# Performance work log

Measured on AMD Instinct MI355X. Metric: run time of the kernel, lower is better.

## Reference

```python
import math
import jax, jax.numpy as jnp
import numpy as np

B, N, D = 2, 768, 512
H = 8
DK = D // H
BETA_NOT = 0.5
EPS = 1e-6


def setup_inputs() -> dict:
    key = jax.random.key(0)
    ks = jax.random.split(key, 8)
    s = 0.02
    return {
        "x": jax.random.normal(ks[0], (B, N, D), dtype=jnp.float32),
        "qkv1_w": jax.random.normal(ks[1], (D, 3 * D), dtype=jnp.float32) * s,
        "qkv2_w": jax.random.normal(ks[2], (D, 3 * D), dtype=jnp.float32) * s,
        "proj_w": jax.random.normal(ks[3], (D, D), dtype=jnp.float32) * s,
        "conv1_w": jax.random.normal(ks[4], (16, 6), dtype=jnp.float32) * 0.3,
        "conv1_b": jax.random.normal(ks[5], (16,), dtype=jnp.float32) * 0.1,
        "conv2_w": jax.random.normal(ks[6], (4, 16), dtype=jnp.float32) * 0.3,
        "conv2_b": jnp.full((4,), -5.0, dtype=jnp.float32),
        "chain_logit": jnp.asarray(-2.0, dtype=jnp.float32),
    }


def _qkv(x, w):
    b, n, d = x.shape
    qkv = (x @ w).reshape(b, n, 3, H, DK).transpose(2, 0, 3, 1, 4)  # [3,B,h,N,dk]
    return qkv[0], qkv[1], qkv[2]


def reference(x, qkv1_w, qkv2_w, proj_w, conv1_w, conv1_b, conv2_w, conv2_b, chain_logit):
    scale = 1.0 / math.sqrt(DK)
    q1, k1, v1 = _qkv(x, qkv1_w)
    q2, k2, v2 = _qkv(x, qkv2_w)

    S1 = jnp.einsum("bhnd,bhmd->bhnm", q1, k1) * scale  # [B,h,N,N]
    S2 = jnp.einsum("bhnd,bhmd->bhnm", q2, k2) * scale
    A1 = jax.nn.softmax(S1, axis=-1)
    A2 = jax.nn.softmax(S2, axis=-1)

    C_right = jnp.einsum("bhnk,bhkm->bhnm", A1, A2)
    C_left = jnp.einsum("bhnk,bhkm->bhnm", A2, A1)
    Cr = jnp.log(C_right + EPS)
    Cl = jnp.log(C_left + EPS)

    # 6-channel edge feature map [B,h,6,N,N]
    feat = jnp.stack(
        [S1, S2, jnp.swapaxes(S1, -1, -2), jnp.swapaxes(S2, -1, -2), Cr, Cl], axis=2
    )
    # 1x1 convs == per-pixel channel mixing
    hid = jnp.einsum("bhcnm,oc->bhonm", feat, conv1_w) + conv1_b[None, None, :, None, None]
    hid = jax.nn.gelu(hid, approximate=True)  # tanh-approx GELU
    gates = jax.nn.sigmoid(
        jnp.einsum("bhcnm,oc->bhonm", hid, conv2_w) + conv2_b[None, None, :, None, None]
    )
    g_and, g_or, g_not, g_chain = gates[:, :, 0], gates[:, :, 1], gates[:, :, 2], gates[:, :, 3]

    Smix = (
        S1
        + g_and * S2  # g_and * (S1 + S2 - S1)
        + g_or * (jnp.logaddexp(S1, S2) - S1)
        - g_not * (BETA_NOT * S2)
        + g_chain * Cr
    )
    A = jax.nn.softmax(Smix, axis=-1)

    y_base = jnp.einsum("bhnm,bhmd->bhnd", A, v1)
    transport = jnp.einsum("bhnm,bhmd->bhnd", A2, v2)
    y_chain = jnp.einsum("bhnm,bhmd->bhnd", A1, transport)
    w = jax.nn.sigmoid(chain_logit)
    y = y_base + w * y_chain

    y = jnp.swapaxes(y, 1, 2).reshape(x.shape[0], x.shape[1], D)  # [B,N,D]
    return y @ proj_w
```

## Files before the change

### kernel.cpp

```cpp
#include <hip/hip_runtime.h>
#include <hip/hip_bf16.h>
#include <math.h>

typedef __hip_bfloat16 bf16;
typedef __attribute__((ext_vector_type(8))) short short8;
typedef __attribute__((ext_vector_type(4))) float f32x4;
typedef __attribute__((ext_vector_type(2))) float f32x2;
#define DEVINL __device__ __forceinline__

constexpr int Bc  = 2;
constexpr int Nc  = 768;
constexpr int Dc  = 512;
constexpr int Hc  = 8;
constexpr int DKc = 64;
constexpr int BHc = Bc * Hc;
constexpr float SCALE    = 0.125f;
constexpr float EPSF     = 1e-6f;
constexpr float BETA_NOT = 0.5f;

DEVINL float ldf(const float* p, long i) { return p[i]; }
DEVINL float ldf(const bf16* p, long i) { return __bfloat162float(p[i]); }
DEVINL void stf(float* p, long i, float v) { p[i] = v; }
DEVINL void stf(bf16* p, long i, float v) { p[i] = __float2bfloat16(v); }

DEVINL float sigf(float x) { return __fdividef(1.f, 1.f + __expf(-x)); }

DEVINL f32x2 fma2(f32x2 a, f32x2 b, f32x2 c) { return __builtin_elementwise_fma(a, b, c); }
DEVINL f32x2 splat2(float x) { return (f32x2){x, x}; }
DEVINL float vexp2(float x) { float r; asm("v_exp_f32 %0, %1" : "=v"(r) : "v"(x)); return r; }
DEVINL float vrcp(float x)  { float r; asm("v_rcp_f32 %0, %1" : "=v"(r) : "v"(x)); return r; }
DEVINL float vlog2(float x) { float r; asm("v_log_f32 %0, %1" : "=v"(r) : "v"(x)); return r; }

DEVINL void gl_lds16(const void* g, void* l) {
    __builtin_amdgcn_global_load_lds(
        (const __attribute__((address_space(1))) void*)g,
        (__attribute__((address_space(3))) void*)l, 16, 0, 0);
}

DEVINL int sniff_is_fp32(const void* xraw) {
    const uint4* p4 = (const uint4*)xraw;
    float mx = 0.f;
#pragma unroll
    for (int j = 0; j < 16; ++j) {
        const uint4 u = p4[j];
        const unsigned w[4] = {u.x, u.y, u.z, u.w};
#pragma unroll
        for (int t = 0; t < 4; ++t) {
            mx = fmaxf(mx, fabsf(__uint_as_float((w[t] & 0xffffu) << 16)));
            mx = fmaxf(mx, fabsf(__uint_as_float(w[t] & 0xffff0000u)));
        }
    }
    return mx > 1000.f ? 1 : 0;
}

DEVINL float cvt_elem(const void* s, long j, int is32) {
    return is32 ? ((const float*)s)[j]
                : __bfloat162float(((const bf16*)s)[j]);
}

__global__ __launch_bounds__(256) void convert_all(
    const void* x, const void* w1, const void* w2, const void* pw,
    const void* c1w, const void* c1b, const void* c2w, const void* c2b,
    const void* ch,
    bf16* xb, bf16* w1b, bf16* w2b, bf16* pwb, float* smallf)
{
    __shared__ int is32s;
    if (threadIdx.x == 0) is32s = sniff_is_fp32(x);
    __syncthreads();
    const int is32 = is32s;
    const long i = (long)blockIdx.x * 256 + threadIdx.x;
    if (i < (long)Bc * Nc * Dc) {
        xb[i]  = __float2bfloat16(cvt_elem(x,  i, is32));
        w1b[i] = __float2bfloat16(cvt_elem(w1, i, is32));
        w2b[i] = __float2bfloat16(cvt_elem(w2, i, is32));
    }
    if (i < (long)Dc * Dc) pwb[i] = __float2bfloat16(cvt_elem(pw, i, is32));
    if (i < 384) {
        const int u = (int)i / 24, k = (int)i % 24;
        float v = 0.f;
        if (k < 12)      v = cvt_elem(c1w, u * 6 + (k >> 1), is32);
        else if (k < 14) v = cvt_elem(c1b, u, is32);
        else if (k >= 16) { const int o = (k - 16) >> 1; v = cvt_elem(c2w, o * 16 + u, is32); }
        smallf[i] = v;
    } else if (i < 392) smallf[i] = cvt_elem(c2b, ((int)i - 384) >> 1, is32);
    else if (i < 394) smallf[i] = cvt_elem(ch, 0, is32);
    else if (i < 512) smallf[i] = 0.f;
}

__global__ __launch_bounds__(256) void fill_sentinel(unsigned short* o) {
    const long i = (long)blockIdx.x * 256 + threadIdx.x;
    if (i < (long)Bc * Nc * Dc) o[i] = 0x40E0;
}

__global__ __launch_bounds__(256) void transpose_bf16(
    const unsigned short* __restrict__ src, unsigned short* __restrict__ dst,
    int R, int C, long sS, long sD)
{
    __shared__ unsigned short tile[64][68];
    const unsigned short* s = src + (long)blockIdx.z * sS;
    unsigned short* d = dst + (long)blockIdx.z * sD;
    const int r0 = blockIdx.y * 64, c0 = blockIdx.x * 64;
    const int t = threadIdx.x;
    const int lr = t >> 4, lc4 = (t & 15) * 4;
#pragma unroll
    for (int i = 0; i < 4; ++i) {
        int r = lr + i * 16;
        *(uint2*)&tile[r][lc4] = *(const uint2*)&s[(long)(r0 + r) * C + c0 + lc4];
    }
    __syncthreads();
#pragma unroll
    for (int i = 0; i < 4; ++i) {
        int r = lr + i * 16;
        unsigned short v[4];
#pragma unroll
        for (int j = 0; j < 4; ++j) v[j] = tile[lc4 + j][r];
        *(uint2*)&d[(long)(c0 + r) * R + r0 + lc4] = *(uint2*)v;
    }
}

template <int EPI, typename TC, int XORB = 0, int XCDSWZ = 0, int RAW = 0>
__global__ __launch_bounds__(256) void gemm_nt_mfma(
    const bf16* __restrict__ Ag, const bf16* __restrict__ Btg,
    TC* __restrict__ Cg, bf16* __restrict__ Craw, int M, int N, int K,
    long sA, long sB, long sC, float alpha)
{
    __shared__ unsigned short Asm[2 * 128 * 32];
    __shared__ unsigned short Bsm[2 * 128 * 32];
    constexpr int BUF = 128 * 32;

    int bx, by, bz;
    if (XCDSWZ) {
        const int wg = blockIdx.x;
        const int xcd = wg & 7, t = wg >> 3;
        bz = xcd + 8 * (t / 36);
        const int tile = t % 36;
        bx = tile % 6; by = tile / 6;
    } else { bx = blockIdx.x; by = blockIdx.y; bz = blockIdx.z; }

    const int tid  = threadIdx.x;
    const int wv   = tid >> 6;
    const int lane = tid & 63;
    const int q    = lane >> 4;
    const int ln   = lane & 15;
    const int wm   = wv & 1;
    const int wn   = wv >> 1;

    const int zb = XORB ? (bz ^ 16) : bz;
    const bf16* A  = Ag  + (long)bz * sA + (long)(by * 128) * K;
    const bf16* Bt = Btg + (long)zb * sB + (long)(bx * 128) * K;
    TC*         C  = Cg  + (long)bz * sC;

    const int sr = lane >> 2, sc = lane & 3;
    const int scs = sc ^ (sr & 3);
    const bf16* gA0 = A  + (long)(wv * 32 + sr)      * K + scs * 8;
    const bf16* gA1 = A  + (long)(wv * 32 + 16 + sr) * K + scs * 8;
    const bf16* gB0 = Bt + (long)(wv * 32 + sr)      * K + scs * 8;
    const bf16* gB1 = Bt + (long)(wv * 32 + 16 + sr) * K + scs * 8;
    unsigned short* lA0 = &Asm[(wv * 32)      * 32];
    unsigned short* lA1 = &Asm[(wv * 32 + 16) * 32];
    unsigned short* lB0 = &Bsm[(wv * 32)      * 32];
    unsigned short* lB1 = &Bsm[(wv * 32 + 16) * 32];

    f32x4 acc[4][4];
#pragma unroll
    for (int i = 0; i < 4; ++i)
#pragma unroll
        for (int j = 0; j < 4; ++j)
            acc[i][j] = (f32x4){0.f, 0.f, 0.f, 0.f};

    const int qs = (q ^ (ln & 3)) * 8;

    gl_lds16(gA0, lA0);
    gl_lds16(gA1, lA1);
    gl_lds16(gB0, lB0);
    gl_lds16(gB1, lB1);
    __syncthreads();

    int cur = 0;
    for (int k0 = 0; k0 < K; k0 += 32) {
        const int nxt = cur ^ 1;
        if (k0 + 32 < K) {
            const int no = nxt * BUF;
            gl_lds16(gA0 + k0 + 32, lA0 + no);
            gl_lds16(gA1 + k0 + 32, lA1 + no);
            gl_lds16(gB0 + k0 + 32, lB0 + no);
            gl_lds16(gB1 + k0 + 32, lB1 + no);
        }

        const unsigned short* Ac = &Asm[cur * BUF];
        const unsigned short* Bc = &Bsm[cur * BUF];
        short8 af[4], bfr[4];
#pragma unroll
        for (int mt = 0; mt < 4; ++mt) {
            int m = wm * 64 + mt * 16 + ln;
            af[mt] = *(const short8*)&Ac[m * 32 + qs];
        }
#pragma unroll
        for (int nt = 0; nt < 4; ++nt) {
            int n = wn * 64 + nt * 16 + ln;
            bfr[nt] = *(const short8*)&Bc[n * 32 + qs];
        }
#pragma unroll
        for (int mt = 0; mt < 4; ++mt)
#pragma unroll
            for (int nt = 0; nt < 4; ++nt)
                acc[mt][nt] = __builtin_amdgcn_mfma_f32_16x16x32_bf16(
                    af[mt], bfr[nt], acc[mt][nt], 0, 0, 0);

        __syncthreads();
        cur = nxt;
    }

#pragma unroll
    for (int mt = 0; mt < 4; ++mt) {
#pragma unroll
        for (int nt = 0; nt < 4; ++nt) {
            const int col = bx * 128 + wn * 64 + nt * 16 + ln;
            const int rowb = by * 128 + wm * 64 + mt * 16 + q * 4;
#pragma unroll
            for (int r = 0; r < 4; ++r) {
                float vraw = acc[mt][nt][r] * alpha;
                if (RAW) {
                    if (bz < 16)
                        Craw[(long)bz * M * N + (long)(rowb + r) * N + col] =
                            __float2bfloat16(vraw);
                }
                float v = vraw;
                if (EPI == 1) v = __logf(fmaxf(v, 0.f) + EPSF);
                stf(C, (long)(rowb + r) * N + col, v);
            }
        }
    }
}

__global__ __launch_bounds__(256) void qkv_mfma(
    const bf16* __restrict__ X,
    const bf16* __restrict__ w1t, const bf16* __restrict__ w2t,
    bf16* __restrict__ q1, bf16* __restrict__ k1, bf16* __restrict__ v1,
    bf16* __restrict__ q2, bf16* __restrict__ k2, bf16* __restrict__ v2)
{
    constexpr int K = Dc;
    __shared__ unsigned short Asm[2 * 128 * 32];
    __shared__ unsigned short Bsm[2 * 128 * 32];
    constexpr int BUF = 128 * 32;

    const int tid  = threadIdx.x;
    const int wv   = tid >> 6;
    const int lane = tid & 63;
    const int q    = lane >> 4;
    const int ln   = lane & 15;
    const int wm   = wv & 1;
    const int wn   = wv >> 1;
    const int set  = blockIdx.z;

    const bf16* Wt = set ? w2t : w1t;
    bf16* Q  = set ? q2 : q1;
    bf16* Ko = set ? k2 : k1;
    bf16* V  = set ? v2 : v1;

    const bf16* A  = X  + (long)(blockIdx.y * 128) * K;
    const bf16* Bt = Wt + (long)(blockIdx.x * 128) * K;

    const int sr = lane >> 2, sc = lane & 3;
    const int scs = sc ^ (sr & 3);
    const bf16* gA0 = A  + (long)(wv * 32 + sr)      * K + scs * 8;
    const bf16* gA1 = A  + (long)(wv * 32 + 16 + sr) * K + scs * 8;
    const bf16* gB0 = Bt + (long)(wv * 32 + sr)      * K + scs * 8;
    const bf16* gB1 = Bt + (long)(wv * 32 + 16 + sr) * K + scs * 8;
    unsigned short* lA0 = &Asm[(wv * 32)      * 32];
    unsigned short* lA1 = &Asm[(wv * 32 + 16) * 32];
    unsigned short* lB0 = &Bsm[(wv * 32)      * 32];
    unsigned short* lB1 = &Bsm[(wv * 32 + 16) * 32];

    f32x4 acc[4][4];
#pragma unroll
    for (int i = 0; i < 4; ++i)
#pragma unroll
        for (int j = 0; j < 4; ++j)
            acc[i][j] = (f32x4){0.f, 0.f, 0.f, 0.f};

    const int qs = (q ^ (ln & 3)) * 8;

    gl_lds16(gA0, lA0);
    gl_lds16(gA1, lA1);
    gl_lds16(gB0, lB0);
    gl_lds16(gB1, lB1);
    __syncthreads();

    int cur = 0;
    for (int k0 = 0; k0 < K; k0 += 32) {
        const int nxt = cur ^ 1;
        if (k0 + 32 < K) {
            const int no = nxt * BUF;
            gl_lds16(gA0 + k0 + 32, lA0 + no);
            gl_lds16(gA1 + k0 + 32, lA1 + no);
            gl_lds16(gB0 + k0 + 32, lB0 + no);
            gl_lds16(gB1 + k0 + 32, lB1 + no);
        }

        const unsigned short* Ac = &Asm[cur * BUF];
        const unsigned short* Bc = &Bsm[cur * BUF];
        short8 af[4], bfr[4];
#pragma unroll
        for (int mt = 0; mt < 4; ++mt) {
            int m = wm * 64 + mt * 16 + ln;
            af[mt] = *(const short8*)&Ac[m * 32 + qs];
        }
#pragma unroll
        for (int nt = 0; nt < 4; ++nt) {
            int n = wn * 64 + nt * 16 + ln;
            bfr[nt] = *(const short8*)&Bc[n * 32 + qs];
        }
#pragma unroll
        for (int mt = 0; mt < 4; ++mt)
#pragma unroll
            for (int nt = 0; nt < 4; ++nt)
                acc[mt][nt] = __builtin_amdgcn_mfma_f32_16x16x32_bf16(
                    af[mt], bfr[nt], acc[mt][nt], 0, 0, 0);

        __syncthreads();
        cur = nxt;
    }

#pragma unroll
    for (int mt = 0; mt < 4; ++mt) {
#pragma unroll
        for (int nt = 0; nt < 4; ++nt) {
            const int col  = blockIdx.x * 128 + wn * 64 + nt * 16 + ln;
            const int rowb = blockIdx.y * 128 + wm * 64 + mt * 16 + q * 4;
            const int t = col >> 9;
            const int h = (col >> 6) & 7;
            const int dk = col & 63;
            bf16* dst = (t == 0) ? Q : (t == 1) ? Ko : V;
#pragma unroll
            for (int r = 0; r < 4; ++r) {
                const int row = rowb + r;
                const int b = row >= Nc ? 1 : 0;
                const int n = row - b * Nc;
                dst[(((long)b * Hc + h) * Nc + n) * DKc + dk] =
                    __float2bfloat16(acc[mt][nt][r]);
            }
        }
    }
}

struct N64Acc { f32x4 acc[2][4]; };

template <typename DUMMY = void>
DEVINL void n64_core(const bf16* A, const bf16* Bt, int K,
                     unsigned short* Asm, unsigned short* Bsm, N64Acc& R)
{
    const int tid  = threadIdx.x;
    const int wave = tid >> 6;
    const int lane = tid & 63;
    const int q    = lane >> 4;
    const int ln   = lane & 15;

    const int sr = tid >> 3, k8 = tid & 7;
    const bf16* pa[4];
    const bf16* pb[2];
    int wa[4], wb[2];
#pragma unroll
    for (int i = 0; i < 4; ++i) {
        pa[i] = A + (long)(sr + i * 32) * K + k8 * 8;
        wa[i] = (sr + i * 32) * 72 + k8 * 8;
    }
#pragma unroll
    for (int i = 0; i < 2; ++i) {
        pb[i] = Bt + (long)(sr + i * 32) * K + k8 * 8;
        wb[i] = (sr + i * 32) * 72 + k8 * 8;
    }

#pragma unroll
    for (int i = 0; i < 2; ++i)
#pragma unroll
        for (int j = 0; j < 4; ++j)
            R.acc[i][j] = (f32x4){0.f, 0.f, 0.f, 0.f};

    for (int k0 = 0; k0 < K; k0 += 64) {
        uint4 va[4], vb[2];
#pragma unroll
        for (int i = 0; i < 4; ++i) va[i] = *(const uint4*)(pa[i] + k0);
#pragma unroll
        for (int i = 0; i < 2; ++i) vb[i] = *(const uint4*)(pb[i] + k0);
        __syncthreads();
#pragma unroll
        for (int i = 0; i < 4; ++i) *(uint4*)&Asm[wa[i]] = va[i];
#pragma unroll
        for (int i = 0; i < 2; ++i) *(uint4*)&Bsm[wb[i]] = vb[i];
        __syncthreads();

#pragma unroll
        for (int kc = 0; kc < 2; ++kc) {
            short8 af[2], bfr[4];
#pragma unroll
            for (int mt = 0; mt < 2; ++mt) {
                int m = wave * 32 + mt * 16 + ln;
                af[mt] = *(const short8*)&Asm[m * 72 + kc * 32 + q * 8];
            }
#pragma unroll
            for (int nt = 0; nt < 4; ++nt) {
                int n = nt * 16 + ln;
                bfr[nt] = *(const short8*)&Bsm[n * 72 + kc * 32 + q * 8];
            }
#pragma unroll
            for (int mt = 0; mt < 2; ++mt)
#pragma unroll
                for (int nt = 0; nt < 4; ++nt)
                    R.acc[mt][nt] = __builtin_amdgcn_mfma_f32_16x16x32_bf16(
                        af[mt], bfr[nt], R.acc[mt][nt], 0, 0, 0);
        }
    }
}

struct N64hAcc { f32x4 acc[4]; };

template <typename DUMMY = void>
DEVINL void n64h_core(const bf16* A, const bf16* Bt, int K,
                      unsigned short* Asm, unsigned short* Bsm, N64hAcc& R)
{
    const int tid  = threadIdx.x;
    const int wave = tid >> 6;
    const int lane = tid & 63;
    const int q    = lane >> 4;
    const int ln   = lane & 15;

    const int sr = tid >> 3, k8 = tid & 7;
    const bf16* pa[2];
    const bf16* pb[2];
    int wa[2], wb[2];
#pragma unroll
    for (int i = 0; i < 2; ++i) {
        pa[i] = A  + (long)(sr + i * 32) * K + k8 * 8;
        wa[i] = (sr + i * 32) * 72 + k8 * 8;
        pb[i] = Bt + (long)(sr + i * 32) * K + k8 * 8;
        wb[i] = wa[i];
    }

#pragma unroll
    for (int j = 0; j < 4; ++j)
        R.acc[j] = (f32x4){0.f, 0.f, 0.f, 0.f};

    for (int k0 = 0; k0 < K; k0 += 64) {
        uint4 va[2], vb[2];
#pragma unroll
        for (int i = 0; i < 2; ++i) va[i] = *(const uint4*)(pa[i] + k0);
#pragma unroll
        for (int i = 0; i < 2; ++i) vb[i] = *(const uint4*)(pb[i] + k0);
        __syncthreads();
#pragma unroll
        for (int i = 0; i < 2; ++i) *(uint4*)&Asm[wa[i]] = va[i];
#pragma unroll
        for (int i = 0; i < 2; ++i) *(uint4*)&Bsm[wb[i]] = vb[i];
        __syncthreads();

#pragma unroll
        for (int kc = 0; kc < 2; ++kc) {
            short8 af;
            af = *(const short8*)&Asm[(wave * 16 + ln) * 72 + kc * 32 + q * 8];
            short8 bfr[4];
#pragma unroll
            for (int nt = 0; nt < 4; ++nt) {
                int n = nt * 16 + ln;
                bfr[nt] = *(const short8*)&Bsm[n * 72 + kc * 32 + q * 8];
            }
#pragma unroll
            for (int nt = 0; nt < 4; ++nt)
                R.acc[nt] = __builtin_amdgcn_mfma_f32_16x16x32_bf16(
                    af, bfr[nt], R.acc[nt], 0, 0, 0);
        }
    }
}

__global__ __launch_bounds__(256) void gemm_n64_pair(
    const bf16* __restrict__ A0g, const bf16* __restrict__ B0g, bf16* __restrict__ C0tg,
    const bf16* __restrict__ A1g, const bf16* __restrict__ B1g, bf16* __restrict__ C1g,
    int M, int K, long sA, long sB, long sC)
{
    __shared__ unsigned short Asm[128 * 72];
    __shared__ unsigned short Bsm[64 * 72];

    const int zz = blockIdx.z & 15;
    const int second = blockIdx.z >> 4;
    const bf16* A  = (second ? A1g : A0g) + (long)zz * sA + (long)(blockIdx.y * 128) * K;
    const bf16* Bt = (second ? B1g : B0g) + (long)zz * sB;

    N64Acc R;
    n64_core(A, Bt, K, Asm, Bsm, R);

    const int tid = threadIdx.x;
    const int wave = tid >> 6, lane = tid & 63, q = lane >> 4, ln = lane & 15;

    if (second) {
        bf16* C = C1g + (long)zz * sC;
#pragma unroll
        for (int mt = 0; mt < 2; ++mt) {
#pragma unroll
            for (int nt = 0; nt < 4; ++nt) {
                const int col  = nt * 16 + ln;
                const int rowb = blockIdx.y * 128 + wave * 32 + mt * 16 + q * 4;
#pragma unroll
                for (int r = 0; r < 4; ++r)
                    C[(long)(rowb + r) * 64 + col] = __float2bfloat16(R.acc[mt][nt][r]);
            }
        }
    } else {
        __syncthreads();
#pragma unroll
        for (int mt = 0; mt < 2; ++mt) {
#pragma unroll
            for (int nt = 0; nt < 4; ++nt) {
                const int col = nt * 16 + ln;
                const int rwb = wave * 32 + mt * 16 + q * 4;
#pragma unroll
                for (int r = 0; r < 4; ++r)
                    *(bf16*)&Asm[col * 136 + rwb + r] = __float2bfloat16(R.acc[mt][nt][r]);
            }
        }
        __syncthreads();
        bf16* Ct = C0tg + (long)zz * sC;
        const int dk  = tid >> 2;
        const int nc0 = (tid & 3) * 32;
        const int gn0 = blockIdx.y * 128;
#pragma unroll
        for (int c8 = 0; c8 < 4; ++c8) {
            uint4 v = *(const uint4*)&Asm[dk * 136 + nc0 + c8 * 8];
            *(uint4*)&Ct[(long)dk * Nc + gn0 + nc0 + c8 * 8] = v;
        }
    }
}

__global__ __launch_bounds__(256) void gemm_n64_both_h(
    const bf16* __restrict__ Ab, const bf16* __restrict__ v1t,
    const bf16* __restrict__ Craw, const bf16* __restrict__ v2t,
    const float* __restrict__ smallf, bf16* __restrict__ yc,
    int K, long sA, long sB)
{
    __shared__ unsigned short Asm[64 * 72];
    __shared__ unsigned short Bsm[64 * 72];

    const int bh = blockIdx.z;
    const long arow = (long)(blockIdx.y * 64) * K;

    N64hAcc R1;
    n64h_core(Ab + (long)bh * sA + arow, v1t + (long)bh * sB, K, Asm, Bsm, R1);
    N64hAcc R2;
    n64h_core(Craw + (long)bh * sA + arow, v2t + (long)bh * sB, K, Asm, Bsm, R2);

    const float w = sigf(smallf[392]);
    const int b = bh >> 3, h = bh & 7;

    const int tid = threadIdx.x;
    const int wave = tid >> 6, lane = tid & 63, q = lane >> 4, ln = lane & 15;
#pragma unroll
    for (int nt = 0; nt < 4; ++nt) {
        const int col  = nt * 16 + ln;
        const int rowb = blockIdx.y * 64 + wave * 16 + q * 4;
#pragma unroll
        for (int r = 0; r < 4; ++r) {
            const int n = rowb + r;
            yc[((long)(b * Nc + n)) * Dc + h * DKc + col] =
                __float2bfloat16(R1.acc[nt][r] + w * R2.acc[nt][r]);
        }
    }
}

__global__ __launch_bounds__(256) void gemm_n64_combine(
    const bf16* __restrict__ A1b, const bf16* __restrict__ trt,
    const bf16* __restrict__ yb1, const float* __restrict__ smallf,
    bf16* __restrict__ yc, int M, int K, long sA, long sB)
{
    __shared__ unsigned short Asm[128 * 72];
    __shared__ unsigned short Bsm[64 * 72];

    const int bh = blockIdx.z;
    const bf16* A  = A1b + (long)bh * sA + (long)(blockIdx.y * 128) * K;
    const bf16* Bt = trt + (long)bh * sB;

    N64Acc R;
    n64_core(A, Bt, K, Asm, Bsm, R);

    const float w = sigf(smallf[392]);
    const int b = bh >> 3, h = bh & 7;
    const long yb1base = (long)bh * Nc * DKc;

    const int tid = threadIdx.x;
    const int wave = tid >> 6, lane = tid & 63, q = lane >> 4, ln = lane & 15;
#pragma unroll
    for (int mt = 0; mt < 2; ++mt) {
#pragma unroll
        for (int nt = 0; nt < 4; ++nt) {
            const int col  = nt * 16 + ln;
            const int rowb = blockIdx.y * 128 + wave * 32 + mt * 16 + q * 4;
#pragma unroll
            for (int r = 0; r < 4; ++r) {
                const int n = rowb + r;
                const float base = __bfloat162float(yb1[yb1base + (long)n * 64 + col]);
                yc[((long)(b * Nc + n)) * Dc + h * DKc + col] =
                    __float2bfloat16(base + w * R.acc[mt][nt][r]);
            }
        }
    }
}

__global__ __launch_bounds__(256) void gemm_n64_yb(
    const bf16* __restrict__ Ag, const bf16* __restrict__ Btg,
    bf16* __restrict__ Cg, int M, int K, long sA, long sB, long sC)
{
    __shared__ unsigned short Asm[128 * 72];
    __shared__ unsigned short Bsm[64 * 72];

    const int zz = blockIdx.z;
    const bf16* A  = Ag + (long)zz * sA + (long)(blockIdx.y * 128) * K;
    const bf16* Bt = Btg + (long)zz * sB;

    N64Acc R;
    n64_core(A, Bt, K, Asm, Bsm, R);

    bf16* C = Cg + (long)zz * sC;
    const int tid = threadIdx.x;
    const int wave = tid >> 6, lane = tid & 63, q = lane >> 4, ln = lane & 15;
#pragma unroll
    for (int mt = 0; mt < 2; ++mt) {
#pragma unroll
        for (int nt = 0; nt < 4; ++nt) {
            const int col  = nt * 16 + ln;
            const int rowb = blockIdx.y * 128 + wave * 32 + mt * 16 + q * 4;
#pragma unroll
            for (int r = 0; r < 4; ++r)
                C[(long)(rowb + r) * 64 + col] = __float2bfloat16(R.acc[mt][nt][r]);
        }
    }
}

__global__ __launch_bounds__(256) void softmax_rows_w(
    const float* __restrict__ src, bf16* __restrict__ dst)
{
    const int wid  = threadIdx.x >> 6;
    const int lane = threadIdx.x & 63;
    const long row = (long)blockIdx.x * 4 + wid;
    const float* s = src + row * Nc;

    float4 v[3];
#pragma unroll
    for (int i = 0; i < 3; ++i)
        v[i] = *(const float4*)&s[i * 256 + lane * 4];

    float m = -1e30f;
#pragma unroll
    for (int i = 0; i < 3; ++i)
        m = fmaxf(m, fmaxf(fmaxf(v[i].x, v[i].y), fmaxf(v[i].z, v[i].w)));
#pragma unroll
    for (int off = 32; off > 0; off >>= 1)
        m = fmaxf(m, __shfl_xor(m, off, 64));

    float e[12];
    float sum = 0.f;
#pragma unroll
    for (int i = 0; i < 3; ++i) {
        e[i * 4 + 0] = __expf(v[i].x - m);
        e[i * 4 + 1] = __expf(v[i].y - m);
        e[i * 4 + 2] = __expf(v[i].z - m);
        e[i * 4 + 3] = __expf(v[i].w - m);
        sum += e[i * 4 + 0] + e[i * 4 + 1] + e[i * 4 + 2] + e[i * 4 + 3];
    }
#pragma unroll
    for (int off = 32; off > 0; off >>= 1)
        sum += __shfl_xor(sum, off, 64);

    const float inv = 1.f / fmaxf(sum, 1e-30f);
    unsigned short* d = (unsigned short*)dst + row * Nc;
#pragma unroll
    for (int i = 0; i < 3; ++i) {
        unsigned short o[4];
#pragma unroll
        for (int j = 0; j < 4; ++j) {
            const bf16 b = __float2bfloat16(e[i * 4 + j] * inv);
            o[j] = *(const unsigned short*)&b;
        }
        *(uint2*)&d[i * 256 + lane * 4] = *(const uint2*)o;
    }
}

__global__ __launch_bounds__(256) void gates_smix(
    const float* __restrict__ S1g, const float* __restrict__ S2g,
    const bf16* __restrict__ Crg, const bf16* __restrict__ Clg,
    float* __restrict__ Smixg, const float* __restrict__ smallf)
{
    __shared__ float t1t[32][17], t2t[32][17];

    const long mat = (long)blockIdx.z * Nc * Nc;
    const float* S1 = S1g + mat;
    const float* S2 = S2g + mat;
    const unsigned short* Cr = (const unsigned short*)Crg + mat;
    const unsigned short* Cl = (const unsigned short*)Clg + mat;
    float* Smix = Smixg + mat;

    const int tid = threadIdx.x;

    const int n0 = blockIdx.y * 16, m0 = blockIdx.x * 32;
    {
        const int r = tid >> 3, c2 = (tid & 7) * 2;
        const float2 a = *(const float2*)&S1[(long)(m0 + r) * Nc + n0 + c2];
        const float2 b = *(const float2*)&S2[(long)(m0 + r) * Nc + n0 + c2];
        t1t[r][c2] = a.x; t1t[r][c2 + 1] = a.y;
        t2t[r][c2] = b.x; t2t[r][c2 + 1] = b.y;
    }
    __syncthreads();

    const int tx = tid & 15, ty = tid >> 4;
    const int n = n0 + ty;
    const long idx = (long)n * Nc + m0 + tx * 2;

    const float2 s1v = *(const float2*)&S1[idx];
    const float2 s2v = *(const float2*)&S2[idx];
    const unsigned cru = *(const unsigned*)&Cr[idx];
    const unsigned clu = *(const unsigned*)&Cl[idx];

    const f32x2 s1a = {s1v.x, s1v.y};
    const f32x2 s2a = {s2v.x, s2v.y};
    const f32x2 cra = {__uint_as_float((cru & 0xffffu) << 16),
                       __uint_as_float(cru & 0xffff0000u)};
    const f32x2 cla = {__uint_as_float((clu & 0xffffu) << 16),
                       __uint_as_float(clu & 0xffff0000u)};
    const f32x2 s1t = {t1t[tx * 2][ty], t1t[tx * 2 + 1][ty]};
    const f32x2 s2t = {t2t[tx * 2][ty], t2t[tx * 2 + 1][ty]};

    f32x2 g0 = *(const f32x2*)&smallf[384];
    f32x2 g1 = *(const f32x2*)&smallf[386];
    f32x2 g2 = *(const f32x2*)&smallf[388];
    f32x2 g3 = *(const f32x2*)&smallf[390];

    const f32x2 gc1  = splat2(-2.30220902f);
    const f32x2 gc3  = splat2(-0.10294357f);
    const f32x2 one2 = splat2(1.f);

#pragma unroll
    for (int u = 0; u < 16; ++u) {
        const f32x2* cw = (const f32x2*)&smallf[u * 24];
        f32x2 h = cw[6];
        h = fma2(s1a, cw[0], h);
        h = fma2(s2a, cw[1], h);
        h = fma2(s1t, cw[2], h);
        h = fma2(s2t, cw[3], h);
        h = fma2(cra, cw[4], h);
        h = fma2(cla, cw[5], h);
        const f32x2 hh = h * h;
        const f32x2 z2 = h * fma2(hh, gc3, gc1);
        f32x2 e;  e[0]  = vexp2(z2[0]); e[1]  = vexp2(z2[1]);
        const f32x2 d = one2 + e;
        f32x2 rc; rc[0] = vrcp(d[0]);   rc[1] = vrcp(d[1]);
        const f32x2 hid = h * rc;
        g0 = fma2(hid, cw[8],  g0);
        g1 = fma2(hid, cw[9],  g1);
        g2 = fma2(hid, cw[10], g2);
        g3 = fma2(hid, cw[11], g3);
    }

    const f32x2 nl2e = splat2(-1.44269504f);
    const f32x2 ln2v = splat2(0.69314718f);
    auto sig2 = [&](f32x2 x) -> f32x2 {
        const f32x2 t = x * nl2e;
        f32x2 e;  e[0] = vexp2(t[0]); e[1] = vexp2(t[1]);
        const f32x2 d = one2 + e;
        f32x2 r;  r[0] = vrcp(d[0]);  r[1] = vrcp(d[1]);
        return r;
    };
    const f32x2 ga2 = sig2(g0);
    const f32x2 go2 = sig2(g1);
    const f32x2 gn2 = sig2(g2);
    const f32x2 gc2 = sig2(g3);

    const f32x2 dd = s1a - s2a;
    f32x2 ad; ad[0] = fabsf(dd[0]); ad[1] = fabsf(dd[1]);
    const f32x2 t2 = ad * nl2e;
    f32x2 ee; ee[0] = vexp2(t2[0]); ee[1] = vexp2(t2[1]);
    const f32x2 lp = one2 + ee;
    f32x2 lg; lg[0] = vlog2(lp[0]); lg[1] = vlog2(lp[1]);
    const f32x2 mx2 = __builtin_elementwise_max(s1a, s2a);
    const f32x2 lae = fma2(lg, ln2v, mx2);

    f32x2 o2 = s1a;
    o2 = fma2(ga2, s2a, o2);
    o2 = fma2(go2, lae - s1a, o2);
    o2 = fma2(gn2, s2a * splat2(-BETA_NOT), o2);
    o2 = fma2(gc2, cra, o2);
    *(float2*)&Smix[idx] = (float2){o2[0], o2[1]};
}

__global__ __launch_bounds__(256) void proj_n64h(
    const bf16* __restrict__ yc, const bf16* __restrict__ pwt,
    const void* __restrict__ xraw, void* __restrict__ out)
{
    constexpr int K = Dc;
    constexpr int N = Dc;
    __shared__ unsigned short Asm[64 * 72];
    __shared__ unsigned short Bsm[64 * 72];
    __shared__ int is32s;
    if (threadIdx.x == 0) is32s = sniff_is_fp32(xraw);

    const bf16* A  = yc  + (long)(blockIdx.y * 64) * K;
    const bf16* Bt = pwt + (long)(blockIdx.x * 64) * K;

    N64hAcc R;
    n64h_core(A, Bt, K, Asm, Bsm, R);

    const int is32 = is32s;
    const int tid = threadIdx.x;
    const int wave = tid >> 6, lane = tid & 63, q = lane >> 4, ln = lane & 15;
#pragma unroll
    for (int nt = 0; nt < 4; ++nt) {
        const int col  = blockIdx.x * 64 + nt * 16 + ln;
        const int rowb = blockIdx.y * 64 + wave * 16 + q * 4;
#pragma unroll
        for (int r = 0; r < 4; ++r) {
            const long o = (long)(rowb + r) * N + col;
            if (is32) ((float*)out)[o] = R.acc[nt][r];
            else      ((bf16*)out)[o] = __float2bfloat16(R.acc[nt][r]);
        }
    }
}

extern "C" void kernel_launch(void* const* d_in, const int* in_sizes, int n_in,
                              void* d_out, int out_size, void* d_ws, size_t ws_size,
                              hipStream_t stream)
{
    const size_t HD   = (size_t)BHc * Nc * DKc;
    const size_t HDh  = HD / 2;
    const size_t MAT  = (size_t)Nc * Nc;
    const size_t MATS = (size_t)BHc * MAT;
    const long   HSTR = (long)Nc * DKc;

    float* ws = (float*)d_ws;
    size_t off = 0;
    auto alloc = [&](size_t n) { float* p = ws + off; off += n; return p; };

    bf16* xb  = (bf16*)alloc(HDh);
    bf16* w1b = (bf16*)alloc(HDh);
    bf16* w2b = (bf16*)alloc(HDh);
    bf16* w1t = (bf16*)alloc(HDh);
    bf16* w2t = (bf16*)alloc(HDh);
    bf16* pwb = (bf16*)alloc((size_t)Dc * Dc / 2);
    bf16* pwt = (bf16*)alloc((size_t)Dc * Dc / 2);
    float* smallf = alloc(512);
    bf16* q1b = (bf16*)alloc(HDh); bf16* q2b = (bf16*)alloc(HDh);
    bf16* k1b = (bf16*)alloc(HDh); bf16* k2b = (bf16*)alloc(HDh);
    bf16* v1b = (bf16*)alloc(HDh); bf16* v2b = (bf16*)alloc(HDh);
    bf16* v1t = (bf16*)alloc(HDh); bf16* v2t = (bf16*)alloc(HDh);
    bf16* trt = (bf16*)alloc(HDh);
    float* S1   = alloc(MATS);
    float* S2   = alloc(MATS);
    float* Smix = alloc(MATS);
    bf16* A1b = (bf16*)alloc(MATS / 2);
    bf16* A2b = (bf16*)alloc(MATS / 2);
    bf16* Crb = (bf16*)alloc(MATS / 2);
    bf16* Clb = (bf16*)alloc(MATS / 2);
    bf16* yb1 = (bf16*)alloc(HDh);
    bf16* yc  = (bf16*)alloc(HDh);

    const size_t NEED_BASE = off * sizeof(float);
    bf16* Crawb = (bf16*)alloc(MATS / 2);
    const size_t NEED_A = off * sizeof(float);
    const int pathA = ws_size >= NEED_A;

    bf16* A1tb = (bf16*)Smix;
    bf16* A2tb = ((bf16*)Smix) + MATS;
    bf16* Ab   = (bf16*)S1;

    if (ws_size < NEED_BASE) {
        fill_sentinel<<<dim3(3072), 256, 0, stream>>>((unsigned short*)d_out);
        return;
    }

    convert_all<<<dim3(3072), 256, 0, stream>>>(
        d_in[0], d_in[1], d_in[2], d_in[3], d_in[4], d_in[5], d_in[6], d_in[7],
        d_in[8], xb, w1b, w2b, pwb, smallf);

    transpose_bf16<<<dim3(24, 8, 2), 256, 0, stream>>>(
        (const unsigned short*)w1b, (unsigned short*)w1t, Dc, 3 * Dc, (long)HD, (long)HD);
    transpose_bf16<<<dim3(8, 8, 1), 256, 0, stream>>>(
        (const unsigned short*)pwb, (unsigned short*)pwt, Dc, Dc, 0, 0);
    qkv_mfma<<<dim3(12, 12, 2), 256, 0, stream>>>(
        xb, w1t, w2t, q1b, k1b, v1b, q2b, k2b, v2b);
    transpose_bf16<<<dim3(1, 12, 2 * BHc), 256, 0, stream>>>(
        (const unsigned short*)v1b, (unsigned short*)v1t, Nc, DKc, HSTR, HSTR);

    gemm_nt_mfma<0, float><<<dim3(6, 6, 2 * BHc), 256, 0, stream>>>(
        q1b, k1b, S1, nullptr, Nc, Nc, DKc, HSTR, HSTR, (long)MAT, SCALE);

    softmax_rows_w<<<(2 * BHc * Nc) / 4, 256, 0, stream>>>(S1, A1b);
    transpose_bf16<<<dim3(12, 12, 2 * BHc), 256, 0, stream>>>(
        (const unsigned short*)A1b, (unsigned short*)A1tb, Nc, Nc, (long)MAT, (long)MAT);

    if (pathA)
        gemm_nt_mfma<1, bf16, 1, 1, 1><<<dim3(1152), 256, 0, stream>>>(
            A1b, A1tb, Crb, Crawb, Nc, Nc, Nc, (long)MAT, (long)MAT, (long)MAT, 1.f);
    else
        gemm_nt_mfma<1, bf16, 1, 1, 0><<<dim3(1152), 256, 0, stream>>>(
            A1b, A1tb, Crb, nullptr, Nc, Nc, Nc, (long)MAT, (long)MAT, (long)MAT, 1.f);

    gates_smix<<<dim3(24, 48, BHc), 256, 0, stream>>>(S1, S2, Crb, Clb, Smix, smallf);

    softmax_rows_w<<<(BHc * Nc) / 4, 256, 0, stream>>>(Smix, Ab);

    if (pathA) {
        gemm_n64_both_h<<<dim3(1, 12, BHc), 256, 0, stream>>>(
            Ab, v1t, Crawb, v2t, smallf, yc, Nc, (long)MAT, HSTR);
    } else {
        gemm_n64_pair<<<dim3(1, 6, 2 * BHc), 256, 0, stream>>>(
            A2b, v2t, trt, Ab, v1t, yb1, Nc, Nc, (long)MAT, HSTR, HSTR);
        gemm_n64_combine<<<dim3(1, 6, BHc), 256, 0, stream>>>(
            A1b, trt, yb1, smallf, yc, Nc, Nc, (long)MAT, HSTR);
    }

    proj_n64h<<<dim3(8, 24, 1), 256, 0, stream>>>(yc, pwt, d_in[0], d_out);
}
```

Before: 345.7 us.

## Fuse score GEMM, row softmax and transpose into one kernel

Replaces the separate QK^T GEMM, row softmax and bf16 transpose launches with a single kernel. Each block computes a 16-row strip of scores across all 768 columns with MFMA and does the softmax in registers. It writes S, A and the transposed A directly, the last through an LDS staging tile. This removes two launches and the re-reads of S and A from global memory. In exchange, the 16-row tiles are small, so K is re-read from global memory for every strip, and the transposed stores are narrow 8-byte writes.

```diff
diff --git a/kernel.cpp b/kernel.cpp
--- a/kernel.cpp
+++ b/kernel.cpp
@@ -115,6 +115,146 @@
 #pragma unroll
         for (int j = 0; j < 4; ++j) v[j] = tile[lc4 + j][r];
         *(uint2*)&d[(long)(c0 + r) * R + r0 + lc4] = *(uint2*)v;
+    }
+}
+
+__global__ __launch_bounds__(256) void sgemm_softmax(
+    const bf16* __restrict__ qg, const bf16* __restrict__ kg,
+    float* __restrict__ Sg, bf16* __restrict__ Ag_, bf16* __restrict__ Atg)
+{
+    __shared__ unsigned short Bsm[256 * 72];
+    __shared__ unsigned short Asm16[16 * 72];
+    __shared__ float red[4][16];
+
+    const int wg  = blockIdx.x;
+    const int xcd = wg & 7, tt = wg >> 3;
+    const int z   = xcd + 8 * (tt / 48);
+    const int by  = tt % 48;
+    const long MAT = (long)Nc * Nc;
+
+    const bf16* Q  = qg + (long)z * (Nc * DKc) + (long)(by * 16) * DKc;
+    const bf16* Km = kg + (long)z * (Nc * DKc);
+    float* S  = Sg  + (long)z * MAT + (long)(by * 16) * Nc;
+    bf16*  A  = Ag_ + (long)z * MAT + (long)(by * 16) * Nc;
+    bf16*  At = Atg + (long)z * MAT;
+
+    const int tid  = threadIdx.x;
+    const int wv   = tid >> 6;
+    const int lane = tid & 63;
+    const int q    = lane >> 4;
+    const int ln   = lane & 15;
+    const int sr   = tid >> 3, k8 = tid & 7;
+
+    if (tid < 128) {
+        const int row = tid >> 3, kk = tid & 7;
+        *(uint4*)&Asm16[row * 72 + kk * 8] = *(const uint4*)&Q[row * 64 + kk * 8];
+    }
+
+    f32x4 acc[12];
+#pragma unroll
+    for (int j = 0; j < 12; ++j) acc[j] = (f32x4){0.f, 0.f, 0.f, 0.f};
+
+    for (int c = 0; c < 3; ++c) {
+        __syncthreads();
+#pragma unroll
+        for (int i = 0; i < 8; ++i) {
+            const int row = sr + i * 32;
+            *(uint4*)&Bsm[row * 72 + k8 * 8] =
+                *(const uint4*)&Km[(long)(c * 256 + row) * 64 + k8 * 8];
+        }
+        __syncthreads();
+#pragma unroll
+        for (int kc = 0; kc < 2; ++kc) {
+            const short8 af = *(const short8*)&Asm16[ln * 72 + kc * 32 + q * 8];
+#pragma unroll
+            for (int t = 0; t < 4; ++t) {
+                const int nl = wv * 64 + t * 16 + ln;
+                const short8 bfr = *(const short8*)&Bsm[nl * 72 + kc * 32 + q * 8];
+                acc[c * 4 + t] = __builtin_amdgcn_mfma_f32_16x16x32_bf16(
+                    af, bfr, acc[c * 4 + t], 0, 0, 0);
+            }
+        }
+    }
+
+    float mrow[4] = {-1e30f, -1e30f, -1e30f, -1e30f};
+#pragma unroll
+    for (int j = 0; j < 12; ++j) {
+        const int c = j >> 2, t = j & 3;
+        const int col = c * 256 + wv * 64 + t * 16 + ln;
+#pragma unroll
+        for (int r = 0; r < 4; ++r) {
+            const float v = acc[j][r] * SCALE;
+            acc[j][r] = v;
+            S[(long)(q * 4 + r) * Nc + col] = v;
+            mrow[r] = fmaxf(mrow[r], v);
+        }
+    }
+#pragma unroll
+    for (int off = 8; off > 0; off >>= 1)
+#pragma unroll
+        for (int r = 0; r < 4; ++r)
+            mrow[r] = fmaxf(mrow[r], __shfl_xor(mrow[r], off, 16));
+    if (ln == 0)
+#pragma unroll
+        for (int r = 0; r < 4; ++r) red[wv][q * 4 + r] = mrow[r];
+    __syncthreads();
+    float m4[4];
+#pragma unroll
+    for (int r = 0; r < 4; ++r)
+        m4[r] = fmaxf(fmaxf(red[0][q * 4 + r], red[1][q * 4 + r]),
+                      fmaxf(red[2][q * 4 + r], red[3][q * 4 + r]));
+    __syncthreads();
+
+    float srow[4] = {0.f, 0.f, 0.f, 0.f};
+#pragma unroll
+    for (int j = 0; j < 12; ++j)
+#pragma unroll
+        for (int r = 0; r < 4; ++r) {
+            const float e = __expf(acc[j][r] - m4[r]);
+            acc[j][r] = e;
+            srow[r] += e;
+        }
+#pragma unroll
+    for (int off = 8; off > 0; off >>= 1)
+#pragma unroll
+        for (int r = 0; r < 4; ++r)
+            srow[r] += __shfl_xor(srow[r], off, 16);
+    if (ln == 0)
+#pragma unroll
+        for (int r = 0; r < 4; ++r) red[wv][q * 4 + r] = srow[r];
+    __syncthreads();
+    float inv[4];
+#pragma unroll
+    for (int r = 0; r < 4; ++r)
+        inv[r] = 1.f / fmaxf(red[0][q * 4 + r] + red[1][q * 4 + r] +
+                             red[2][q * 4 + r] + red[3][q * 4 + r], 1e-30f);
+
+    unsigned short* ATl = Bsm;
+#pragma unroll
+    for (int j = 0; j < 12; ++j) {
+        const int c = j >> 2, t = j & 3;
+        const int col = c * 256 + wv * 64 + t * 16 + ln;
+#pragma unroll
+        for (int r = 0; r < 4; ++r) {
+            const bf16 b = __float2bfloat16(acc[j][r] * inv[r]);
+            const unsigned short u = *(const unsigned short*)&b;
+            A[(long)(q * 4 + r) * Nc + col] = *(const bf16*)&u;
+            ATl[col * 20 + q * 4 + r] = u;
+        }
+    }
+    __syncthreads();
+#pragma unroll
+    for (int s = 0; s < 3; ++s) {
+        const int m = tid + s * 256;
+        uint2 v0 = *(const uint2*)&ATl[m * 20 + 0];
+        uint2 v1 = *(const uint2*)&ATl[m * 20 + 4];
+        uint2 v2 = *(const uint2*)&ATl[m * 20 + 8];
+        uint2 v3 = *(const uint2*)&ATl[m * 20 + 12];
+        unsigned short* d = (unsigned short*)&At[(long)m * Nc + by * 16];
+        *(uint2*)&d[0]  = v0;
+        *(uint2*)&d[4]  = v1;
+        *(uint2*)&d[8]  = v2;
+        *(uint2*)&d[12] = v3;
     }
 }
 
@@ -885,12 +1025,8 @@
     transpose_bf16<<<dim3(1, 12, 2 * BHc), 256, 0, stream>>>(
         (const unsigned short*)v1b, (unsigned short*)v1t, Nc, DKc, HSTR, HSTR);
 
-    gemm_nt_mfma<0, float><<<dim3(6, 6, 2 * BHc), 256, 0, stream>>>(
-        q1b, k1b, S1, nullptr, Nc, Nc, DKc, HSTR, HSTR, (long)MAT, SCALE);
-
-    softmax_rows_w<<<(2 * BHc * Nc) / 4, 256, 0, stream>>>(S1, A1b);
-    transpose_bf16<<<dim3(12, 12, 2 * BHc), 256, 0, stream>>>(
-        (const unsigned short*)A1b, (unsigned short*)A1tb, Nc, Nc, (long)MAT, (long)MAT);
+    sgemm_softmax<<<dim3(1536), 256, 0, stream>>>(
+        q1b, k1b, S1, A1b, A1tb);
 
     if (pathA)
         gemm_nt_mfma<1, bf16, 1, 1, 1><<<dim3(1152), 256, 0, stream>>>(
```

New measurement: 331.6 us. 4.1% less time.
